# Performance work log

Hardware: AMD Instinct MI355X
Metric: run time of the kernel (lower is better)

The kernel has to match this reference:

```python
import jax, jax.numpy as jnp
import numpy as np

B, T_ENC, C, H, NSTEPS, NCLS, NEMB = 512, 64, 512, 512, 26, 97, 256


def setup_inputs() -> dict:
    key = jax.random.key(0)
    ks = jax.random.split(key, 20)
    w = lambda k, shape, s=0.05: jax.random.normal(k, shape, dtype=jnp.float32) * s
    return {
        "batch_H": jax.random.normal(ks[0], (B, T_ENC, C), dtype=jnp.float32),
        "Attentive_Sequence": jax.random.normal(ks[1], (B, NSTEPS, H), dtype=jnp.float32),
        "text": jax.random.randint(ks[2], (B, NSTEPS), 0, NCLS),
        "W_i2h": w(ks[3], (H, C)),                      # i2h, bias=False
        "W_h2h": w(ks[4], (H, H)), "b_h2h": w(ks[5], (H,)),
        "w_score": w(ks[6], (H,)),                      # score Linear(H,1), bias=False
        "W_ih": w(ks[7], (4 * H, C + NEMB)), "W_hh": w(ks[8], (4 * H, H)),
        "b_ih": w(ks[9], (4 * H,)), "b_hh": w(ks[10], (4 * H,)),
        "Wf1": w(ks[11], (H, H)), "bf1": w(ks[12], (H,)),   # GatedBimodal branch 1
        "Wf2": w(ks[13], (H, H)), "bf2": w(ks[14], (H,)),   # GatedBimodal branch 2
        "Wz": w(ks[15], (H, 2 * H)), "bz": w(ks[16], (H,)),  # gate over concat
        "W_gen": w(ks[17], (NCLS, H)), "b_gen": w(ks[18], (NCLS,)),
        "emb_table": w(ks[19], (NCLS + 1, NEMB), 1.0),
    }


def reference(batch_H, Attentive_Sequence, text, W_i2h, W_h2h, b_h2h, w_score,
              W_ih, W_hh, b_ih, b_hh, Wf1, bf1, Wf2, bf2, Wz, bz,
              W_gen, b_gen, emb_table):
    b = batch_H.shape[0]
    char_embs = emb_table[text]                                  # [B, NSTEPS, NEMB]
    H_proj = jnp.einsum('btc,hc->bth', batch_H, W_i2h)           # i2h once (loop-invariant)
    h0 = jnp.zeros((b, H), jnp.float32)
    c0 = jnp.zeros((b, H), jnp.float32)

    def step(carry, xs):
        h, c = carry
        emb_t, seq_t = xs                                        # [B,NEMB], [B,H]
        hp = h @ W_h2h.T + b_h2h                                 # h2h
        e = jnp.tanh(H_proj + hp[:, None, :]) @ w_score          # [B, T_ENC]
        alpha = jax.nn.softmax(e, axis=1)
        context = jnp.einsum('bt,btc->bc', alpha, batch_H)       # bmm(alpha^T, H)
        # GatedBimodal fusion
        f1 = jnp.tanh(context @ Wf1.T + bf1)
        f2 = jnp.tanh(seq_t @ Wf2.T + bf2)
        z = jax.nn.sigmoid(jnp.concatenate([context, seq_t], axis=1) @ Wz.T + bz)
        I_char = z * f1 + (1.0 - z) * f2
        # LSTMCell
        x = jnp.concatenate([I_char, emb_t], axis=1)
        gates = x @ W_ih.T + b_ih + h @ W_hh.T + b_hh
        i_g, f_g, g_g, o_g = jnp.split(gates, 4, axis=1)
        c_new = jax.nn.sigmoid(f_g) * c + jax.nn.sigmoid(i_g) * jnp.tanh(g_g)
        h_new = jax.nn.sigmoid(o_g) * jnp.tanh(c_new)
        return (h_new, c_new), (h_new, alpha, I_char)

    xs = (jnp.swapaxes(char_embs, 0, 1), jnp.swapaxes(Attentive_Sequence, 0, 1))
    _, (hs, alphas, chars) = jax.lax.scan(step, (h0, c0), xs)
    output_hiddens = jnp.swapaxes(hs, 0, 1)                      # [B, NSTEPS, H]
    seq_attention_map = jnp.transpose(alphas, (1, 2, 0))         # [B, T_ENC, NSTEPS]
    Char = jnp.swapaxes(chars, 0, 1)                             # [B, NSTEPS, H]
    probs = output_hiddens @ W_gen.T + b_gen                     # [B, NSTEPS, NCLS]
    return probs, seq_attention_map, output_hiddens, Char
```

## Files before the change

### kernel.cpp

```cpp
#include <hip/hip_runtime.h>

#define NS_ 26
#define NCLS_ 97

typedef short bf16x8 __attribute__((ext_vector_type(8)));
typedef float f32x4 __attribute__((ext_vector_type(4)));

__device__ __forceinline__ unsigned short f2bf(float f) {
  union { float f; unsigned u; } v; v.f = f;
  unsigned r = v.u + 0x7fffu + ((v.u >> 16) & 1u);
  return (unsigned short)(r >> 16);
}
__device__ __forceinline__ float bf2f(unsigned short h) {
  union { unsigned u; float f; } v; v.u = ((unsigned)h) << 16;
  return v.f;
}
__device__ __forceinline__ float sigm_f(float x) { return 1.f / (1.f + __expf(-x)); }
__device__ __forceinline__ float tanh_f(float x) { return 1.f - 2.f / (1.f + __expf(2.f * x)); }

__device__ __forceinline__ void gl_lds16(const void* g, void* l) {
  __builtin_amdgcn_global_load_lds(
      (const __attribute__((address_space(1))) unsigned int*)g,
      (__attribute__((address_space(3))) unsigned int*)l, 16, 0, 0);
}

template <bool OUTF>
__global__ __launch_bounds__(256) void gemm_tiled_k(
    const unsigned short* __restrict__ Ag, const unsigned short* __restrict__ Bg,
    const float* __restrict__ bias, float* __restrict__ outF,
    unsigned short* __restrict__ outB, int K, long ldo, int Nvalid) {
  __shared__ unsigned short As[128 * 64];
  __shared__ unsigned short Bs[128 * 64];
  const int tid = threadIdx.x;
  const int w = tid >> 6, l = tid & 63;
  const int l15 = l & 15, lq = l >> 4;
  const int wm = w >> 1, wn = w & 1;
  const long rowBase = (long)blockIdx.y * 128;
  const long colBase = (long)blockIdx.x * 128;
  const int lrow = l >> 3, ps_st = l & 7;
  f32x4 acc[4][4] = {};
  for (int kt = 0; kt < K; kt += 64) {
#pragma unroll
    for (int i = 0; i < 4; ++i) {
      const int row = i * 32 + w * 8 + lrow;
      const int ls = ps_st ^ (row & 7);
      gl_lds16(Ag + (rowBase + row) * K + kt + ls * 8, As + i * 2048 + w * 512);
      gl_lds16(Bg + (colBase + row) * K + kt + ls * 8, Bs + i * 2048 + w * 512);
    }
    __syncthreads();
#pragma unroll
    for (int kh = 0; kh < 2; ++kh) {
      bf16x8 af[4], bfr[4];
#pragma unroll
      for (int mi = 0; mi < 4; ++mi) {
        const int row = wm * 64 + mi * 16 + l15;
        const int ps = (kh * 4 + lq) ^ (row & 7);
        af[mi] = *(const bf16x8*)(As + row * 64 + ps * 8);
      }
#pragma unroll
      for (int ni = 0; ni < 4; ++ni) {
        const int row = wn * 64 + ni * 16 + l15;
        const int ps = (kh * 4 + lq) ^ (row & 7);
        bfr[ni] = *(const bf16x8*)(Bs + row * 64 + ps * 8);
      }
#pragma unroll
      for (int mi = 0; mi < 4; ++mi)
#pragma unroll
        for (int ni = 0; ni < 4; ++ni)
          acc[mi][ni] = __builtin_amdgcn_mfma_f32_16x16x32_bf16(af[mi], bfr[ni], acc[mi][ni], 0, 0, 0);
    }
    __syncthreads();
  }
#pragma unroll
  for (int mi = 0; mi < 4; ++mi)
#pragma unroll
    for (int ni = 0; ni < 4; ++ni) {
      const long gcol = colBase + wn * 64 + ni * 16 + l15;
      if (gcol >= Nvalid) continue;
      const float bv = bias ? bias[gcol] : 0.f;
#pragma unroll
      for (int r = 0; r < 4; ++r) {
        const long grow = rowBase + wm * 64 + mi * 16 + lq * 4 + r;
        const float v = acc[mi][ni][r] + bv;
        if (OUTF) outF[grow * ldo + gcol] = v;
        else      outB[grow * ldo + gcol] = f2bf(v);
      }
    }
}

__global__ __launch_bounds__(512, 4) void attn_fused_k(
    const unsigned short* __restrict__ hrd, const unsigned short* __restrict__ Wt4,
    const float* __restrict__ b_h2h, const unsigned short* __restrict__ Hproj,
    const unsigned short* __restrict__ bH, const float* __restrict__ w_score,
    float* __restrict__ attn_map, unsigned short* __restrict__ ctx, int s) {
  const int b = blockIdx.x, tid = threadIdx.x;
  __shared__ float hs[512];
  __shared__ float hp_t[520];
  __shared__ float ws_t[520];
  __shared__ float e_s[64];
  __shared__ float csum[512];
  hs[tid] = bf2f(hrd[(long)b * 512 + tid]);
  ws_t[(tid & 7) * 65 + (tid >> 3)] = w_score[tid];
  __syncthreads();
  {
    float acc = b_h2h[tid];
    const unsigned short* wp = Wt4 + tid * 4;
#pragma unroll 4
    for (int k4 = 0; k4 < 128; ++k4) {
      const ushort4 wv = *(const ushort4*)(wp + k4 * 2048);
      const f32x4 hv = *(const f32x4*)(hs + k4 * 4);
      acc += bf2f(wv.x) * hv[0] + bf2f(wv.y) * hv[1]
           + bf2f(wv.z) * hv[2] + bf2f(wv.w) * hv[3];
    }
    hp_t[(tid & 7) * 65 + (tid >> 3)] = acc;
  }
  __syncthreads();
  const int w8 = tid >> 6, l = tid & 63;
#pragma unroll
  for (int tt = 0; tt < 8; ++tt) {
    const int t = w8 * 8 + tt;
    const bf16x8 hv = *(const bf16x8*)(Hproj + ((long)b * 64 + t) * 512 + l * 8);
    float acc = 0.f;
#pragma unroll
    for (int j = 0; j < 8; ++j)
      acc += tanh_f(bf2f((unsigned short)hv[j]) + hp_t[j * 65 + l]) * ws_t[j * 65 + l];
    acc += __shfl_xor(acc, 1);
    acc += __shfl_xor(acc, 2);
    acc += __shfl_xor(acc, 4);
    acc += __shfl_xor(acc, 8);
    acc += __shfl_xor(acc, 16);
    acc += __shfl_xor(acc, 32);
    if (l == 0) e_s[t] = acc;
  }
  __syncthreads();
  if (tid < 64) {
    const float e = e_s[tid];
    float m = e;
    for (int off = 32; off; off >>= 1) m = fmaxf(m, __shfl_xor(m, off));
    const float p = __expf(e - m);
    float sum = p;
    for (int off = 32; off; off >>= 1) sum += __shfl_xor(sum, off);
    const float a = p / sum;
    e_s[tid] = a;
    attn_map[((long)b * 64 + tid) * NS_ + s] = a;
  }
  __syncthreads();
  const int half = tid >> 8, jj = tid & 255;
  float c0 = 0.f, c1 = 0.f;
  const unsigned* bhp = (const unsigned*)(bH + ((long)b * 64 + half * 32) * 512) + jj;
#pragma unroll 8
  for (int t = 0; t < 32; ++t) {
    const float a = e_s[half * 32 + t];
    const unsigned pv = bhp[(long)t * 256];
    c0 += a * bf2f((unsigned short)(pv & 0xffffu));
    c1 += a * bf2f((unsigned short)(pv >> 16));
  }
  if (half) { csum[jj * 2] = c0; csum[jj * 2 + 1] = c1; }
  __syncthreads();
  if (!half) {
    c0 += csum[jj * 2];
    c1 += csum[jj * 2 + 1];
    ((unsigned*)ctx)[(long)b * 256 + jj] = (unsigned)f2bf(c0) | ((unsigned)f2bf(c1) << 16);
  }
}

__global__ __launch_bounds__(512, 4) void gated_fused_k(
    const unsigned short* __restrict__ ctx, const unsigned short* __restrict__ Wfz,
    const unsigned short* __restrict__ FZpre, const float* __restrict__ bf1,
    unsigned short* __restrict__ Ichar, float* __restrict__ Char_out, int s) {
  __shared__ float ls[2 * 16 * 65];
  const int tid = threadIdx.x, w = tid >> 6, l = tid & 63, l15 = l & 15, lq = l >> 4;
  const int b0 = blockIdx.y * 16, j0 = blockIdx.x * 64;
  const int which = w >> 2, nh = w & 3;
  f32x4 acc = {};
  const long arow = b0 + l15;
  const long gw = (long)(which ? 512 : 0) + j0 + nh * 16 + l15;
  for (int kt = 0; kt < 512; kt += 64) {
    const int k0 = kt + lq * 8, k1 = k0 + 32;
    const bf16x8 a0 = *(const bf16x8*)(ctx + arow * 512 + k0);
    const bf16x8 a1 = *(const bf16x8*)(ctx + arow * 512 + k1);
    const bf16x8 w0 = *(const bf16x8*)(Wfz + gw * 512 + k0);
    const bf16x8 w1 = *(const bf16x8*)(Wfz + gw * 512 + k1);
    acc = __builtin_amdgcn_mfma_f32_16x16x32_bf16(a0, w0, acc, 0, 0, 0);
    acc = __builtin_amdgcn_mfma_f32_16x16x32_bf16(a1, w1, acc, 0, 0, 0);
  }
#pragma unroll
  for (int r = 0; r < 4; ++r)
    ls[which * 1040 + (lq * 4 + r) * 65 + nh * 16 + l15] = acc[r];
  __syncthreads();
#pragma unroll
  for (int i = 0; i < 2; ++i) {
    const int e = tid + i * 512;
    const int r = e >> 6, c = e & 63;
    const long b = b0 + r;
    const int j = j0 + c;
    const float f1 = tanh_f(ls[r * 65 + c] + bf1[j]);
    const float zc = ls[1040 + r * 65 + c];
    const long pr = (b * NS_ + s) * 1024;
    const float f2 = tanh_f(bf2f(FZpre[pr + j]));
    const float z = sigm_f(zc + bf2f(FZpre[pr + 512 + j]));
    const float I = z * f1 + (1.f - z) * f2;
    Char_out[(b * NS_ + s) * 512 + j] = I;
    Ichar[b * 512 + j] = f2bf(I);
  }
}

__global__ __launch_bounds__(512, 4) void gates_lstm_k(
    const unsigned short* __restrict__ Ichar, const unsigned short* __restrict__ embb,
    const unsigned short* __restrict__ hrd, const unsigned short* __restrict__ Wihh,
    const float* __restrict__ biasG, float* __restrict__ cbuf,
    float* __restrict__ hid_out, unsigned short* __restrict__ hwr, int s) {
  __shared__ float gs[4 * 32 * 33];
  const int tid = threadIdx.x, w = tid >> 6, l = tid & 63, l15 = l & 15, lq = l >> 4;
  const int b0 = blockIdx.y * 32, j0 = blockIdx.x * 32;
  const int g = w & 3, mi = w >> 2;
  const long arow = b0 + mi * 16 + l15;
  f32x4 acc[2] = {};
  for (int kt = 0; kt < 1280; kt += 64) {
    const int k0 = kt + lq * 8, k1 = k0 + 32;
    bf16x8 a0, a1, b0r[2], b1r[2];
    if (kt < 512) {
      a0 = *(const bf16x8*)(Ichar + arow * 512 + k0);
      a1 = *(const bf16x8*)(Ichar + arow * 512 + k1);
    } else if (kt < 768) {
      a0 = *(const bf16x8*)(embb + (arow * NS_ + s) * 256 + (k0 - 512));
      a1 = *(const bf16x8*)(embb + (arow * NS_ + s) * 256 + (k1 - 512));
    } else {
      a0 = *(const bf16x8*)(hrd + arow * 512 + (k0 - 768));
      a1 = *(const bf16x8*)(hrd + arow * 512 + (k1 - 768));
    }
#pragma unroll
    for (int ni = 0; ni < 2; ++ni) {
      const long wrow = (long)g * 512 + j0 + ni * 16 + l15;
      b0r[ni] = *(const bf16x8*)(Wihh + wrow * 1280 + k0);
      b1r[ni] = *(const bf16x8*)(Wihh + wrow * 1280 + k1);
    }
#pragma unroll
    for (int ni = 0; ni < 2; ++ni) {
      acc[ni] = __builtin_amdgcn_mfma_f32_16x16x32_bf16(a0, b0r[ni], acc[ni], 0, 0, 0);
      acc[ni] = __builtin_amdgcn_mfma_f32_16x16x32_bf16(a1, b1r[ni], acc[ni], 0, 0, 0);
    }
  }
#pragma unroll
  for (int ni = 0; ni < 2; ++ni)
#pragma unroll
    for (int r = 0; r < 4; ++r) {
      const int rl = mi * 16 + lq * 4 + r;
      const int cl = ni * 16 + l15;
      gs[(g * 32 + rl) * 33 + cl] = acc[ni][r];
    }
  __syncthreads();
#pragma unroll
  for (int i = 0; i < 2; ++i) {
    const int e = tid + i * 512;
    const int r = e >> 5, c = e & 31;
    const long b = b0 + r;
    const int j = j0 + c;
    const float ig = sigm_f(gs[(0 * 32 + r) * 33 + c] + biasG[j]);
    const float fg = sigm_f(gs[(1 * 32 + r) * 33 + c] + biasG[512 + j]);
    const float gg = tanh_f(gs[(2 * 32 + r) * 33 + c] + biasG[1024 + j]);
    const float og = sigm_f(gs[(3 * 32 + r) * 33 + c] + biasG[1536 + j]);
    const float cn = fg * cbuf[b * 512 + j] + ig * gg;
    cbuf[b * 512 + j] = cn;
    const float h = og * tanh_f(cn);
    hid_out[(b * NS_ + s) * 512 + j] = h;
    hwr[b * 512 + j] = f2bf(h);
  }
}

__global__ __launch_bounds__(256) void probs_k(
    const float* __restrict__ Af, const unsigned short* __restrict__ Wg,
    const float* __restrict__ bias, float* __restrict__ outp) {
  const int tid = threadIdx.x, w = tid >> 6, l = tid & 63, l15 = l & 15, lq = l >> 4;
  const long mrow = (long)blockIdx.y * 64 + w * 16 + l15;
  const int nbase = blockIdx.x * 64;
  f32x4 acc[4] = {};
  for (int kt = 0; kt < 512; kt += 32) {
    const int k = kt + lq * 8;
    const float4 av0 = *(const float4*)(Af + mrow * 512 + k);
    const float4 av1 = *(const float4*)(Af + mrow * 512 + k + 4);
    bf16x8 a;
    a[0] = (short)f2bf(av0.x); a[1] = (short)f2bf(av0.y);
    a[2] = (short)f2bf(av0.z); a[3] = (short)f2bf(av0.w);
    a[4] = (short)f2bf(av1.x); a[5] = (short)f2bf(av1.y);
    a[6] = (short)f2bf(av1.z); a[7] = (short)f2bf(av1.w);
#pragma unroll
    for (int nb = 0; nb < 4; ++nb) {
      const bf16x8 b = *(const bf16x8*)(Wg + (long)(nbase + nb * 16 + l15) * 512 + k);
      acc[nb] = __builtin_amdgcn_mfma_f32_16x16x32_bf16(a, b, acc[nb], 0, 0, 0);
    }
  }
#pragma unroll
  for (int nb = 0; nb < 4; ++nb) {
    const int colg = nbase + nb * 16 + l15;
    if (colg >= NCLS_) continue;
    const float bv = bias[colg];
#pragma unroll
    for (int r = 0; r < 4; ++r) {
      const long rowg = (long)blockIdx.y * 64 + w * 16 + lq * 4 + r;
      outp[rowg * NCLS_ + colg] = acc[nb][r] + bv;
    }
  }
}

__global__ void cvt_f32_bf16_k(const float* __restrict__ in, unsigned short* __restrict__ out, long n) {
  const long i = ((long)blockIdx.x * 256 + threadIdx.x) * 4;
  if (i + 4 <= n) {
    const float4 v = *(const float4*)(in + i);
    ushort4 o;
    o.x = f2bf(v.x); o.y = f2bf(v.y); o.z = f2bf(v.z); o.w = f2bf(v.w);
    *(ushort4*)(out + i) = o;
  }
}

__global__ void embed_k(const float* __restrict__ emb_table, const int* __restrict__ text,
                        unsigned short* __restrict__ out) {
  const int bs = blockIdx.x, j = threadIdx.x;
  const int t = text[bs];
  out[(long)bs * 256 + j] = f2bf(emb_table[(long)t * 256 + j]);
}

__global__ void pack_Wt4_k(const float* __restrict__ W, unsigned short* __restrict__ out) {
  const long idx = (long)blockIdx.x * 256 + threadIdx.x;
  const int j = (int)(idx >> 9), k = (int)(idx & 511);
  out[((long)(k >> 2) * 2048) + j * 4 + (k & 3)] = f2bf(W[idx]);
}

__global__ void pack_Wihh_k(const float* __restrict__ W_ih, const float* __restrict__ W_hh,
                            unsigned short* __restrict__ out) {
  const long idx = (long)blockIdx.x * 256 + threadIdx.x;
  const int row = (int)(idx / 1280), c = (int)(idx % 1280);
  const float v = (c < 768) ? W_ih[(long)row * 768 + c] : W_hh[(long)row * 512 + (c - 768)];
  out[idx] = f2bf(v);
}

__global__ void pack_wfz_k(const float* __restrict__ Wf, const float* __restrict__ Wz, int zoff,
                           unsigned short* __restrict__ out) {
  const long idx = (long)blockIdx.x * 256 + threadIdx.x;
  const int row = (int)(idx >> 9), k = (int)(idx & 511);
  const float v = (row < 512) ? Wf[(long)row * 512 + k]
                              : Wz[(long)(row - 512) * 1024 + zoff + k];
  out[idx] = f2bf(v);
}

__global__ void pack_Wgen_k(const float* __restrict__ W_gen, unsigned short* __restrict__ out) {
  const long idx = (long)blockIdx.x * 256 + threadIdx.x;
  const int row = (int)(idx >> 9), k = (int)(idx & 511);
  out[idx] = (row < NCLS_) ? f2bf(W_gen[(long)row * 512 + k]) : (unsigned short)0;
}

__global__ void pack_bias_k(const float* __restrict__ b_ih, const float* __restrict__ b_hh,
                            const float* __restrict__ bf2, const float* __restrict__ bz,
                            float* __restrict__ biasG, float* __restrict__ biasFZ) {
  const int i = blockIdx.x * 256 + threadIdx.x;
  if (i < 2048) {
    biasG[i] = b_ih[i] + b_hh[i];
  } else {
    const int j = i - 2048;
    biasFZ[j] = (j < 512) ? bf2[j] : bz[j - 512];
  }
}

extern "C" void kernel_launch(void* const* d_in, const int* in_sizes, int n_in,
                              void* d_out, int out_size, void* d_ws, size_t ws_size,
                              hipStream_t stream) {
  (void)in_sizes; (void)n_in; (void)out_size; (void)ws_size;
  const float* batch_H  = (const float*)d_in[0];
  const float* AS       = (const float*)d_in[1];
  const int*   text     = (const int*)d_in[2];
  const float* W_i2h    = (const float*)d_in[3];
  const float* W_h2h    = (const float*)d_in[4];
  const float* b_h2h    = (const float*)d_in[5];
  const float* w_score  = (const float*)d_in[6];
  const float* W_ih     = (const float*)d_in[7];
  const float* W_hh     = (const float*)d_in[8];
  const float* b_ih     = (const float*)d_in[9];
  const float* b_hh     = (const float*)d_in[10];
  const float* Wf1      = (const float*)d_in[11];
  const float* bf1      = (const float*)d_in[12];
  const float* Wf2      = (const float*)d_in[13];
  const float* bf2      = (const float*)d_in[14];
  const float* Wz       = (const float*)d_in[15];
  const float* bz       = (const float*)d_in[16];
  const float* W_gen    = (const float*)d_in[17];
  const float* b_gen    = (const float*)d_in[18];
  const float* emb_tab  = (const float*)d_in[19];

  float* out = (float*)d_out;
  float* out_probs = out;
  float* out_attn  = out + 1291264;
  float* out_hid   = out + 2143232;
  float* out_char  = out + 8958976;

  char* wsp = (char*)d_ws;
  auto alloc = [&](size_t bytes) { char* p = wsp; wsp += (bytes + 255) & ~(size_t)255; return p; };
  unsigned short* bH    = (unsigned short*)alloc(33554432);
  unsigned short* Hproj = (unsigned short*)alloc(33554432);
  unsigned short* ASb   = (unsigned short*)alloc(13631488);
  unsigned short* embb  = (unsigned short*)alloc(6815744);
  unsigned short* FZpre = (unsigned short*)alloc(27262976);
  unsigned short* Wt4   = (unsigned short*)alloc(524288);
  unsigned short* Wfz   = (unsigned short*)alloc(1048576);
  unsigned short* Wfz2  = (unsigned short*)alloc(1048576);
  unsigned short* Wihh  = (unsigned short*)alloc(5242880);
  unsigned short* Wgenb = (unsigned short*)alloc(131072);
  unsigned short* Wi2hb = (unsigned short*)alloc(524288);
  float* biasG          = (float*)alloc(8192);
  float* biasFZ         = (float*)alloc(4096);
  char* ab = (char*)ASb;
  unsigned short* ctx   = (unsigned short*)(ab);
  unsigned short* Ichar = (unsigned short*)(ab + 524288);
  float* cbuf           = (float*)(ab + 1048576);
  unsigned short* hbuf  = (unsigned short*)(ab + 2097152);

  cvt_f32_bf16_k<<<dim3(16384), dim3(256), 0, stream>>>(batch_H, bH, 16777216);
  cvt_f32_bf16_k<<<dim3(6656), dim3(256), 0, stream>>>(AS, ASb, 6815744);
  cvt_f32_bf16_k<<<dim3(256), dim3(256), 0, stream>>>(W_i2h, Wi2hb, 262144);
  embed_k<<<dim3(13312), dim3(256), 0, stream>>>(emb_tab, text, embb);
  pack_Wt4_k<<<dim3(1024), dim3(256), 0, stream>>>(W_h2h, Wt4);
  pack_Wihh_k<<<dim3(10240), dim3(256), 0, stream>>>(W_ih, W_hh, Wihh);
  pack_wfz_k<<<dim3(2048), dim3(256), 0, stream>>>(Wf1, Wz, 0, Wfz);
  pack_wfz_k<<<dim3(2048), dim3(256), 0, stream>>>(Wf2, Wz, 512, Wfz2);
  pack_Wgen_k<<<dim3(256), dim3(256), 0, stream>>>(W_gen, Wgenb);
  pack_bias_k<<<dim3(12), dim3(256), 0, stream>>>(b_ih, b_hh, bf2, bz, biasG, biasFZ);

  gemm_tiled_k<false><<<dim3(4, 256), dim3(256), 0, stream>>>(
      bH, Wi2hb, nullptr, nullptr, Hproj, 512, 512, 512);

  gemm_tiled_k<false><<<dim3(8, 104), dim3(256), 0, stream>>>(
      ASb, Wfz2, biasFZ, nullptr, FZpre, 512, 1024, 1024);

  hipMemsetAsync(cbuf, 0, 1048576, stream);
  hipMemsetAsync(hbuf, 0, 1048576, stream);

  for (int s = 0; s < NS_; ++s) {
    unsigned short* hrd = hbuf + (s & 1) * 262144;
    unsigned short* hwr = hbuf + ((s + 1) & 1) * 262144;
    attn_fused_k<<<dim3(512), dim3(512), 0, stream>>>(
        hrd, Wt4, b_h2h, Hproj, bH, w_score, out_attn, ctx, s);
    gated_fused_k<<<dim3(8, 32), dim3(512), 0, stream>>>(
        ctx, Wfz, FZpre, bf1, Ichar, out_char, s);
    gates_lstm_k<<<dim3(16, 16), dim3(512), 0, stream>>>(
        Ichar, embb, hrd, Wihh, biasG, cbuf, out_hid, hwr, s);
  }

  probs_k<<<dim3(2, 208), dim3(256), 0, stream>>>(out_hid, Wgenb, b_gen, out_probs);
}
```

Before: 1.967 ms.

## Process two batch rows per attention block and merge prep kernels

The attention kernel now uses 1024-thread blocks that each handle two batch rows, so the W_h2h weight stream is shared across two rows and half as many blocks are launched. The ten conversion and packing prep kernels are merged into two flat mega-kernels to cut launch count. The GEMM-style loops in the gated and LSTM-gate kernels are fully unrolled, with pointer arithmetic hoisted out of the loop. The larger blocks may lower occupancy and lengthen each block's serial h2h matvec, and a __syncthreads inside a uniform scope is kept.

```diff
diff --git a/kernel.cpp b/kernel.cpp
--- a/kernel.cpp
+++ b/kernel.cpp
@@ -88,79 +88,89 @@
     }
 }
 
-__global__ __launch_bounds__(512, 4) void attn_fused_k(
+__global__ __launch_bounds__(1024, 4) void attn_fused_k(
     const unsigned short* __restrict__ hrd, const unsigned short* __restrict__ Wt4,
     const float* __restrict__ b_h2h, const unsigned short* __restrict__ Hproj,
     const unsigned short* __restrict__ bH, const float* __restrict__ w_score,
     float* __restrict__ attn_map, unsigned short* __restrict__ ctx, int s) {
-  const int b = blockIdx.x, tid = threadIdx.x;
-  __shared__ float hs[512];
-  __shared__ float hp_t[520];
+  const long b0 = (long)blockIdx.x * 2;
+  const int tid = threadIdx.x;
+  __shared__ float hs[1024];
+  __shared__ float hp_t[1040];
   __shared__ float ws_t[520];
-  __shared__ float e_s[64];
-  __shared__ float csum[512];
-  hs[tid] = bf2f(hrd[(long)b * 512 + tid]);
-  ws_t[(tid & 7) * 65 + (tid >> 3)] = w_score[tid];
+  __shared__ float e_s[128];
+  __shared__ float csum[1024];
+  hs[tid] = bf2f(hrd[b0 * 512 + tid]);
+  if (tid < 512) ws_t[(tid & 7) * 65 + (tid >> 3)] = w_score[tid];
   __syncthreads();
   {
-    float acc = b_h2h[tid];
-    const unsigned short* wp = Wt4 + tid * 4;
-#pragma unroll 4
+    const int pair = tid >> 9, j = tid & 511;
+    float acc = b_h2h[j];
+    const unsigned short* wp = Wt4 + j * 4;
+    const float* hv0 = hs + pair * 512;
+#pragma unroll 8
     for (int k4 = 0; k4 < 128; ++k4) {
       const ushort4 wv = *(const ushort4*)(wp + k4 * 2048);
-      const f32x4 hv = *(const f32x4*)(hs + k4 * 4);
+      const f32x4 hv = *(const f32x4*)(hv0 + k4 * 4);
       acc += bf2f(wv.x) * hv[0] + bf2f(wv.y) * hv[1]
            + bf2f(wv.z) * hv[2] + bf2f(wv.w) * hv[3];
     }
-    hp_t[(tid & 7) * 65 + (tid >> 3)] = acc;
-  }
-  __syncthreads();
-  const int w8 = tid >> 6, l = tid & 63;
+    hp_t[pair * 520 + (j & 7) * 65 + (j >> 3)] = acc;
+  }
+  __syncthreads();
+  const int w16 = tid >> 6, l = tid & 63;
+  const int srow = w16 >> 3;
+  const float* hpT = hp_t + srow * 520;
 #pragma unroll
   for (int tt = 0; tt < 8; ++tt) {
-    const int t = w8 * 8 + tt;
-    const bf16x8 hv = *(const bf16x8*)(Hproj + ((long)b * 64 + t) * 512 + l * 8);
+    const int t = (w16 & 7) * 8 + tt;
+    const bf16x8 hv = *(const bf16x8*)(Hproj + ((b0 + srow) * 64 + t) * 512 + l * 8);
     float acc = 0.f;
 #pragma unroll
     for (int j = 0; j < 8; ++j)
-      acc += tanh_f(bf2f((unsigned short)hv[j]) + hp_t[j * 65 + l]) * ws_t[j * 65 + l];
+      acc += tanh_f(bf2f((unsigned short)hv[j]) + hpT[j * 65 + l]) * ws_t[j * 65 + l];
     acc += __shfl_xor(acc, 1);
     acc += __shfl_xor(acc, 2);
     acc += __shfl_xor(acc, 4);
     acc += __shfl_xor(acc, 8);
     acc += __shfl_xor(acc, 16);
     acc += __shfl_xor(acc, 32);
-    if (l == 0) e_s[t] = acc;
-  }
-  __syncthreads();
-  if (tid < 64) {
-    const float e = e_s[tid];
+    if (l == 0) e_s[srow * 64 + t] = acc;
+  }
+  __syncthreads();
+  if ((w16 & 7) == 0) {
+    const int row = w16 >> 3;
+    const float e = e_s[row * 64 + l];
     float m = e;
     for (int off = 32; off; off >>= 1) m = fmaxf(m, __shfl_xor(m, off));
     const float p = __expf(e - m);
     float sum = p;
     for (int off = 32; off; off >>= 1) sum += __shfl_xor(sum, off);
     const float a = p / sum;
-    e_s[tid] = a;
-    attn_map[((long)b * 64 + tid) * NS_ + s] = a;
-  }
-  __syncthreads();
-  const int half = tid >> 8, jj = tid & 255;
-  float c0 = 0.f, c1 = 0.f;
-  const unsigned* bhp = (const unsigned*)(bH + ((long)b * 64 + half * 32) * 512) + jj;
+    e_s[row * 64 + l] = a;
+    attn_map[((b0 + row) * 64 + l) * NS_ + s] = a;
+  }
+  __syncthreads();
+  {
+    const int row = tid >> 9, st = tid & 511;
+    const int half = st >> 8, jj = st & 255;
+    float c0 = 0.f, c1 = 0.f;
+    const unsigned* bhp = (const unsigned*)(bH + ((b0 + row) * 64 + half * 32) * 512) + jj;
+    const float* al = e_s + row * 64 + half * 32;
 #pragma unroll 8
-  for (int t = 0; t < 32; ++t) {
-    const float a = e_s[half * 32 + t];
-    const unsigned pv = bhp[(long)t * 256];
-    c0 += a * bf2f((unsigned short)(pv & 0xffffu));
-    c1 += a * bf2f((unsigned short)(pv >> 16));
-  }
-  if (half) { csum[jj * 2] = c0; csum[jj * 2 + 1] = c1; }
-  __syncthreads();
-  if (!half) {
-    c0 += csum[jj * 2];
-    c1 += csum[jj * 2 + 1];
-    ((unsigned*)ctx)[(long)b * 256 + jj] = (unsigned)f2bf(c0) | ((unsigned)f2bf(c1) << 16);
+    for (int t = 0; t < 32; ++t) {
+      const float a = al[t];
+      const unsigned pv = bhp[(long)t * 256];
+      c0 += a * bf2f((unsigned short)(pv & 0xffffu));
+      c1 += a * bf2f((unsigned short)(pv >> 16));
+    }
+    if (half) { csum[row * 512 + jj * 2] = c0; csum[row * 512 + jj * 2 + 1] = c1; }
+    __syncthreads();
+    if (!half) {
+      c0 += csum[row * 512 + jj * 2];
+      c1 += csum[row * 512 + jj * 2 + 1];
+      ((unsigned*)ctx)[(b0 + row) * 256 + jj] = (unsigned)f2bf(c0) | ((unsigned)f2bf(c1) << 16);
+    }
   }
 }
 
@@ -175,6 +185,7 @@
   f32x4 acc = {};
   const long arow = b0 + l15;
   const long gw = (long)(which ? 512 : 0) + j0 + nh * 16 + l15;
+#pragma unroll
   for (int kt = 0; kt < 512; kt += 64) {
     const int k0 = kt + lq * 8, k1 = k0 + 32;
     const bf16x8 a0 = *(const bf16x8*)(ctx + arow * 512 + k0);
@@ -215,25 +226,25 @@
   const int b0 = blockIdx.y * 32, j0 = blockIdx.x * 32;
   const int g = w & 3, mi = w >> 2;
   const long arow = b0 + mi * 16 + l15;
+  const unsigned short* iptr = Ichar + arow * 512;
+  const unsigned short* eptr = embb + (arow * NS_ + s) * 256 - 512;
+  const unsigned short* hptr = hrd + arow * 512 - 768;
+  const unsigned short* wptr = Wihh + ((long)g * 512 + j0 + l15) * 1280;
   f32x4 acc[2] = {};
+#pragma unroll
   for (int kt = 0; kt < 1280; kt += 64) {
     const int k0 = kt + lq * 8, k1 = k0 + 32;
     bf16x8 a0, a1, b0r[2], b1r[2];
-    if (kt < 512) {
-      a0 = *(const bf16x8*)(Ichar + arow * 512 + k0);
-      a1 = *(const bf16x8*)(Ichar + arow * 512 + k1);
-    } else if (kt < 768) {
-      a0 = *(const bf16x8*)(embb + (arow * NS_ + s) * 256 + (k0 - 512));
-      a1 = *(const bf16x8*)(embb + (arow * NS_ + s) * 256 + (k1 - 512));
-    } else {
-      a0 = *(const bf16x8*)(hrd + arow * 512 + (k0 - 768));
-      a1 = *(const bf16x8*)(hrd + arow * 512 + (k1 - 768));
-    }
+    a0 = (k0 < 512) ? *(const bf16x8*)(iptr + k0)
+       : (k0 < 768) ? *(const bf16x8*)(eptr + k0)
+                    : *(const bf16x8*)(hptr + k0);
+    a1 = (k1 < 512) ? *(const bf16x8*)(iptr + k1)
+       : (k1 < 768) ? *(const bf16x8*)(eptr + k1)
+                    : *(const bf16x8*)(hptr + k1);
 #pragma unroll
     for (int ni = 0; ni < 2; ++ni) {
-      const long wrow = (long)g * 512 + j0 + ni * 16 + l15;
-      b0r[ni] = *(const bf16x8*)(Wihh + wrow * 1280 + k0);
-      b1r[ni] = *(const bf16x8*)(Wihh + wrow * 1280 + k1);
+      b0r[ni] = *(const bf16x8*)(wptr + (long)ni * 16 * 1280 + k0);
+      b1r[ni] = *(const bf16x8*)(wptr + (long)ni * 16 * 1280 + k1);
     }
 #pragma unroll
     for (int ni = 0; ni < 2; ++ni) {
@@ -303,61 +314,93 @@
   }
 }
 
-__global__ void cvt_f32_bf16_k(const float* __restrict__ in, unsigned short* __restrict__ out, long n) {
-  const long i = ((long)blockIdx.x * 256 + threadIdx.x) * 4;
-  if (i + 4 <= n) {
-    const float4 v = *(const float4*)(in + i);
-    ushort4 o;
-    o.x = f2bf(v.x); o.y = f2bf(v.y); o.z = f2bf(v.z); o.w = f2bf(v.w);
-    *(ushort4*)(out + i) = o;
-  }
-}
-
-__global__ void embed_k(const float* __restrict__ emb_table, const int* __restrict__ text,
-                        unsigned short* __restrict__ out) {
-  const int bs = blockIdx.x, j = threadIdx.x;
-  const int t = text[bs];
-  out[(long)bs * 256 + j] = f2bf(emb_table[(long)t * 256 + j]);
-}
-
-__global__ void pack_Wt4_k(const float* __restrict__ W, unsigned short* __restrict__ out) {
-  const long idx = (long)blockIdx.x * 256 + threadIdx.x;
-  const int j = (int)(idx >> 9), k = (int)(idx & 511);
-  out[((long)(k >> 2) * 2048) + j * 4 + (k & 3)] = f2bf(W[idx]);
-}
-
-__global__ void pack_Wihh_k(const float* __restrict__ W_ih, const float* __restrict__ W_hh,
-                            unsigned short* __restrict__ out) {
-  const long idx = (long)blockIdx.x * 256 + threadIdx.x;
-  const int row = (int)(idx / 1280), c = (int)(idx % 1280);
-  const float v = (c < 768) ? W_ih[(long)row * 768 + c] : W_hh[(long)row * 512 + (c - 768)];
-  out[idx] = f2bf(v);
-}
-
-__global__ void pack_wfz_k(const float* __restrict__ Wf, const float* __restrict__ Wz, int zoff,
-                           unsigned short* __restrict__ out) {
-  const long idx = (long)blockIdx.x * 256 + threadIdx.x;
-  const int row = (int)(idx >> 9), k = (int)(idx & 511);
-  const float v = (row < 512) ? Wf[(long)row * 512 + k]
-                              : Wz[(long)(row - 512) * 1024 + zoff + k];
-  out[idx] = f2bf(v);
-}
-
-__global__ void pack_Wgen_k(const float* __restrict__ W_gen, unsigned short* __restrict__ out) {
-  const long idx = (long)blockIdx.x * 256 + threadIdx.x;
-  const int row = (int)(idx >> 9), k = (int)(idx & 511);
-  out[idx] = (row < NCLS_) ? f2bf(W_gen[(long)row * 512 + k]) : (unsigned short)0;
-}
-
-__global__ void pack_bias_k(const float* __restrict__ b_ih, const float* __restrict__ b_hh,
-                            const float* __restrict__ bf2, const float* __restrict__ bz,
-                            float* __restrict__ biasG, float* __restrict__ biasFZ) {
-  const int i = blockIdx.x * 256 + threadIdx.x;
-  if (i < 2048) {
-    biasG[i] = b_ih[i] + b_hh[i];
-  } else {
-    const int j = i - 2048;
-    biasFZ[j] = (j < 512) ? bf2[j] : bz[j - 512];
+#define CVT_N0 4194304L
+#define CVT_N1 1703936L
+#define CVT_N2 65536L
+__global__ void mega_cvt_k(const float* __restrict__ batch_H, const float* __restrict__ AS,
+                           const float* __restrict__ W_i2h,
+                           unsigned short* __restrict__ bH, unsigned short* __restrict__ ASb,
+                           unsigned short* __restrict__ Wi2hb) {
+  const long q = (long)blockIdx.x * 256 + threadIdx.x;
+  const float* src; unsigned short* dst; long i;
+  if (q < CVT_N0) { src = batch_H; dst = bH; i = q; }
+  else if (q < CVT_N0 + CVT_N1) { src = AS; dst = ASb; i = q - CVT_N0; }
+  else if (q < CVT_N0 + CVT_N1 + CVT_N2) { src = W_i2h; dst = Wi2hb; i = q - CVT_N0 - CVT_N1; }
+  else return;
+  const float4 v = *(const float4*)(src + i * 4);
+  ushort4 o;
+  o.x = f2bf(v.x); o.y = f2bf(v.y); o.z = f2bf(v.z); o.w = f2bf(v.w);
+  *(ushort4*)(dst + i * 4) = o;
+}
+
+#define PK_N0 2621440L
+#define PK_N1 524288L
+#define PK_N2 524288L
+#define PK_N3 65536L
+#define PK_N4 262144L
+#define PK_N5 3072L
+#define PK_N6 3407872L
+__global__ void mega_pack_k(
+    const float* __restrict__ W_ih, const float* __restrict__ W_hh,
+    const float* __restrict__ Wf1, const float* __restrict__ Wf2,
+    const float* __restrict__ Wz, const float* __restrict__ W_gen,
+    const float* __restrict__ W_h2h,
+    const float* __restrict__ b_ih, const float* __restrict__ b_hh,
+    const float* __restrict__ bf2, const float* __restrict__ bz,
+    const float* __restrict__ emb_table, const int* __restrict__ text,
+    unsigned short* __restrict__ Wihh, unsigned short* __restrict__ Wfz,
+    unsigned short* __restrict__ Wfz2, unsigned short* __restrict__ Wgenb,
+    unsigned short* __restrict__ Wt4, float* __restrict__ biasG,
+    float* __restrict__ biasFZ, unsigned short* __restrict__ embb) {
+  long q = (long)blockIdx.x * 256 + threadIdx.x;
+  if (q < PK_N0) {
+    const int row = (int)(q / 1280), c = (int)(q % 1280);
+    const float v = (c < 768) ? W_ih[(long)row * 768 + c] : W_hh[(long)row * 512 + (c - 768)];
+    Wihh[q] = f2bf(v);
+    return;
+  }
+  q -= PK_N0;
+  if (q < PK_N1) {
+    const int row = (int)(q >> 9), k = (int)(q & 511);
+    const float v = (row < 512) ? Wf1[(long)row * 512 + k] : Wz[(long)(row - 512) * 1024 + k];
+    Wfz[q] = f2bf(v);
+    return;
+  }
+  q -= PK_N1;
+  if (q < PK_N2) {
+    const int row = (int)(q >> 9), k = (int)(q & 511);
+    const float v = (row < 512) ? Wf2[(long)row * 512 + k]
+                                : Wz[(long)(row - 512) * 1024 + 512 + k];
+    Wfz2[q] = f2bf(v);
+    return;
+  }
+  q -= PK_N2;
+  if (q < PK_N3) {
+    const int row = (int)(q >> 9), k = (int)(q & 511);
+    Wgenb[q] = (row < NCLS_) ? f2bf(W_gen[(long)row * 512 + k]) : (unsigned short)0;
+    return;
+  }
+  q -= PK_N3;
+  if (q < PK_N4) {
+    const int j = (int)(q >> 9), k = (int)(q & 511);
+    Wt4[((long)(k >> 2) * 2048) + j * 4 + (k & 3)] = f2bf(W_h2h[q]);
+    return;
+  }
+  q -= PK_N4;
+  if (q < PK_N5) {
+    if (q < 2048) biasG[q] = b_ih[q] + b_hh[q];
+    else {
+      const int j = (int)(q - 2048);
+      biasFZ[j] = (j < 512) ? bf2[j] : bz[j - 512];
+    }
+    return;
+  }
+  q -= PK_N5;
+  if (q < PK_N6) {
+    const long bs = q >> 8;
+    const int j = (int)(q & 255);
+    const int t = text[bs];
+    embb[q] = f2bf(emb_table[(long)t * 256 + j]);
   }
 }
 
@@ -413,16 +456,10 @@
   float* cbuf           = (float*)(ab + 1048576);
   unsigned short* hbuf  = (unsigned short*)(ab + 2097152);
 
-  cvt_f32_bf16_k<<<dim3(16384), dim3(256), 0, stream>>>(batch_H, bH, 16777216);
-  cvt_f32_bf16_k<<<dim3(6656), dim3(256), 0, stream>>>(AS, ASb, 6815744);
-  cvt_f32_bf16_k<<<dim3(256), dim3(256), 0, stream>>>(W_i2h, Wi2hb, 262144);
-  embed_k<<<dim3(13312), dim3(256), 0, stream>>>(emb_tab, text, embb);
-  pack_Wt4_k<<<dim3(1024), dim3(256), 0, stream>>>(W_h2h, Wt4);
-  pack_Wihh_k<<<dim3(10240), dim3(256), 0, stream>>>(W_ih, W_hh, Wihh);
-  pack_wfz_k<<<dim3(2048), dim3(256), 0, stream>>>(Wf1, Wz, 0, Wfz);
-  pack_wfz_k<<<dim3(2048), dim3(256), 0, stream>>>(Wf2, Wz, 512, Wfz2);
-  pack_Wgen_k<<<dim3(256), dim3(256), 0, stream>>>(W_gen, Wgenb);
-  pack_bias_k<<<dim3(12), dim3(256), 0, stream>>>(b_ih, b_hh, bf2, bz, biasG, biasFZ);
+  mega_cvt_k<<<dim3(23297), dim3(256), 0, stream>>>(batch_H, AS, W_i2h, bH, ASb, Wi2hb);
+  mega_pack_k<<<dim3(28960), dim3(256), 0, stream>>>(
+      W_ih, W_hh, Wf1, Wf2, Wz, W_gen, W_h2h, b_ih, b_hh, bf2, bz, emb_tab, text,
+      Wihh, Wfz, Wfz2, Wgenb, Wt4, biasG, biasFZ, embb);
 
   gemm_tiled_k<false><<<dim3(4, 256), dim3(256), 0, stream>>>(
       bH, Wi2hb, nullptr, nullptr, Hproj, 512, 512, 512);
@@ -436,7 +473,7 @@
   for (int s = 0; s < NS_; ++s) {
     unsigned short* hrd = hbuf + (s & 1) * 262144;
     unsigned short* hwr = hbuf + ((s + 1) & 1) * 262144;
-    attn_fused_k<<<dim3(512), dim3(512), 0, stream>>>(
+    attn_fused_k<<<dim3(256), dim3(1024), 0, stream>>>(
         hrd, Wt4, b_h2h, Hproj, bH, w_score, out_attn, ctx, s);
     gated_fused_k<<<dim3(8, 32), dim3(512), 0, stream>>>(
         ctx, Wfz, FZpre, bf1, Ichar, out_char, s);
```

After: 2.010 ms. +2.2%, slower.
